# Optimization experiments

Hardware: AMD Instinct MI355X
Metric: run time of the kernel (lower is better)

The kernel has to match this reference:

```python
import jax, jax.numpy as jnp
import numpy as np

N_RAYS = 131072
N_SAMPLES = 128
FAR_DIST = 1e10  # matches tf constant 10000000000.0


def setup_inputs() -> dict:
    key = jax.random.key(0)
    k1, k2, k3, k4 = jax.random.split(key, 4)
    density = jax.random.normal(k1, (N_RAYS, N_SAMPLES), dtype=jnp.float32)
    color = jax.random.uniform(k2, (N_RAYS, N_SAMPLES, 3), dtype=jnp.float32)
    z_vals = jax.random.uniform(k3, (N_RAYS, N_SAMPLES), dtype=jnp.float32)
    rays_d = jax.random.normal(k4, (N_RAYS, 3), dtype=jnp.float32)
    return {"density": density, "color": color, "z_vals": z_vals, "rays_d": rays_d}


def reference(density, color, z_vals, rays_d):
    # dists between consecutive samples, last one padded with a huge value
    dists = z_vals[..., 1:] - z_vals[..., :-1]                      # [R, S-1]
    dists = jnp.concatenate(
        [dists, jnp.full_like(dists[..., :1], FAR_DIST)], axis=-1)  # [R, S]
    # scale by ray direction norm (broadcast over samples)
    dists = dists * jnp.linalg.norm(rays_d, axis=-1, keepdims=True)  # [R, S]
    # raw_noise_std = 0 -> no noise added (deterministic)
    alpha = 1.0 - jnp.exp(-jax.nn.relu(density) * dists)             # [R, S]
    # exclusive cumprod of transmittance
    t = jnp.cumprod(1.0 - alpha + 1e-10, axis=-1)                    # [R, S]
    trans = jnp.concatenate(
        [jnp.ones_like(t[..., :1]), t[..., :-1]], axis=-1)           # [R, S]
    weights = alpha * trans                                          # [R, S]
    rgb = jnp.sum(weights[..., None] * color, axis=-2)               # [R, 3]
    return rgb
```

## Files before the change

kernel.cpp:

```cpp
#include <hip/hip_runtime.h>

#define NS 128
#define FAR_DIST 1e10f

__global__ __launch_bounds__(256) void nerf_render_kernel(
    const float* __restrict__ density,
    const float* __restrict__ color,
    const float* __restrict__ z_vals,
    const float* __restrict__ rays_d,
    float* __restrict__ out,
    int n_rays)
{
    const int lane = threadIdx.x & 63;
    const int wave = threadIdx.x >> 6;
    const int ray  = blockIdx.x * 4 + wave;
    if (ray >= n_rays) return;

    const float* drow = density + (size_t)ray * NS;
    const float* zrow = z_vals  + (size_t)ray * NS;
    const float* crow = color   + (size_t)ray * NS * 3;

    float2 d2  = *reinterpret_cast<const float2*>(drow + 2 * lane);
    float2 z2  = *reinterpret_cast<const float2*>(zrow + 2 * lane);
    float2 c01 = *reinterpret_cast<const float2*>(crow + 6 * lane);
    float2 c23 = *reinterpret_cast<const float2*>(crow + 6 * lane + 2);
    float2 c45 = *reinterpret_cast<const float2*>(crow + 6 * lane + 4);

    float dx = rays_d[ray * 3 + 0];
    float dy = rays_d[ray * 3 + 1];
    float dz = rays_d[ray * 3 + 2];
    float nrm = sqrtf(dx * dx + dy * dy + dz * dz);

    float z_next = __shfl_down(z2.x, 1, 64);
    float dist0 = (z2.y - z2.x) * nrm;
    float dist1 = ((lane == 63) ? FAR_DIST : (z_next - z2.y)) * nrm;

    float a0 = 1.0f - expf(-fmaxf(d2.x, 0.0f) * dist0);
    float a1 = 1.0f - expf(-fmaxf(d2.y, 0.0f) * dist1);
    float f0 = 1.0f - a0 + 1e-10f;
    float f1 = 1.0f - a1 + 1e-10f;

    float p = f0 * f1;
    #pragma unroll
    for (int off = 1; off < 64; off <<= 1) {
        float up = __shfl_up(p, off, 64);
        if (lane >= off) p *= up;
    }
    float excl = __shfl_up(p, 1, 64);
    if (lane == 0) excl = 1.0f;

    float w0 = a0 * excl;
    float w1 = a1 * excl * f0;

    float r = w0 * c01.x + w1 * c23.y;
    float g = w0 * c01.y + w1 * c45.x;
    float b = w0 * c23.x + w1 * c45.y;

    #pragma unroll
    for (int off = 32; off >= 1; off >>= 1) {
        r += __shfl_xor(r, off, 64);
        g += __shfl_xor(g, off, 64);
        b += __shfl_xor(b, off, 64);
    }

    if (lane == 0) {
        out[ray * 3 + 0] = r;
        out[ray * 3 + 1] = g;
        out[ray * 3 + 2] = b;
    }
}

extern "C" void kernel_launch(void* const* d_in, const int* in_sizes, int n_in,
                              void* d_out, int out_size, void* d_ws, size_t ws_size,
                              hipStream_t stream) {
    const float* density = (const float*)d_in[0];
    const float* color   = (const float*)d_in[1];
    const float* z_vals  = (const float*)d_in[2];
    const float* rays_d  = (const float*)d_in[3];
    float* out = (float*)d_out;

    const int n_rays = in_sizes[3] / 3;
    const int blocks = (n_rays + 3) / 4;
    hipLaunchKernelGGL(nerf_render_kernel, dim3(blocks), dim3(256), 0, stream,
                       density, color, z_vals, rays_d, out, n_rays);
}
```

Before: 59.10 us.

## Use float4 loads with 32-lane groups per ray and fast exp

Each ray is now handled by a 32-lane group instead of a full 64-lane wave. Each lane processes four samples through float4 loads of density, z and color, so a block of 256 threads covers eight rays. The product scan and the reduction shrink to five shuffle steps, and expf is replaced with __expf. This cuts shuffle overhead and the number of memory instructions for a bandwidth-bound kernel, at the cost of lower-precision exponentials.

```diff
diff --git a/kernel.cpp b/kernel.cpp
--- a/kernel.cpp
+++ b/kernel.cpp
@@ -4,66 +4,73 @@
 #define FAR_DIST 1e10f
 
 __global__ __launch_bounds__(256) void nerf_render_kernel(
-    const float* __restrict__ density,
-    const float* __restrict__ color,
-    const float* __restrict__ z_vals,
-    const float* __restrict__ rays_d,
+    const float4* __restrict__ density4,
+    const float4* __restrict__ color4,
+    const float4* __restrict__ z4,
+    const float*  __restrict__ rays_d,
     float* __restrict__ out,
     int n_rays)
 {
-    const int lane = threadIdx.x & 63;
-    const int wave = threadIdx.x >> 6;
-    const int ray  = blockIdx.x * 4 + wave;
+    const int l   = threadIdx.x & 31;
+    const int grp = threadIdx.x >> 5;
+    const int ray = blockIdx.x * 8 + grp;
     if (ray >= n_rays) return;
 
-    const float* drow = density + (size_t)ray * NS;
-    const float* zrow = z_vals  + (size_t)ray * NS;
-    const float* crow = color   + (size_t)ray * NS * 3;
+    const float4 d  = density4[(size_t)ray * 32 + l];
+    const float4 z  = z4      [(size_t)ray * 32 + l];
+    const size_t cb = (size_t)ray * 96 + 3 * l;
+    const float4 c0 = color4[cb + 0];
+    const float4 c1 = color4[cb + 1];
+    const float4 c2 = color4[cb + 2];
 
-    float2 d2  = *reinterpret_cast<const float2*>(drow + 2 * lane);
-    float2 z2  = *reinterpret_cast<const float2*>(zrow + 2 * lane);
-    float2 c01 = *reinterpret_cast<const float2*>(crow + 6 * lane);
-    float2 c23 = *reinterpret_cast<const float2*>(crow + 6 * lane + 2);
-    float2 c45 = *reinterpret_cast<const float2*>(crow + 6 * lane + 4);
+    const float dx = rays_d[ray * 3 + 0];
+    const float dy = rays_d[ray * 3 + 1];
+    const float dz = rays_d[ray * 3 + 2];
+    const float nrm = sqrtf(dx * dx + dy * dy + dz * dz);
 
-    float dx = rays_d[ray * 3 + 0];
-    float dy = rays_d[ray * 3 + 1];
-    float dz = rays_d[ray * 3 + 2];
-    float nrm = sqrtf(dx * dx + dy * dy + dz * dz);
+    const float zn = __shfl_down(z.x, 1, 32);
+    const float dist0 = (z.y - z.x) * nrm;
+    const float dist1 = (z.z - z.y) * nrm;
+    const float dist2 = (z.w - z.z) * nrm;
+    const float dist3 = ((l == 31) ? FAR_DIST : (zn - z.w)) * nrm;
 
-    float z_next = __shfl_down(z2.x, 1, 64);
-    float dist0 = (z2.y - z2.x) * nrm;
-    float dist1 = ((lane == 63) ? FAR_DIST : (z_next - z2.y)) * nrm;
+    const float e0 = __expf(-fmaxf(d.x, 0.0f) * dist0);
+    const float e1 = __expf(-fmaxf(d.y, 0.0f) * dist1);
+    const float e2 = __expf(-fmaxf(d.z, 0.0f) * dist2);
+    const float e3 = __expf(-fmaxf(d.w, 0.0f) * dist3);
+    const float f0 = e0 + 1e-10f, f1 = e1 + 1e-10f;
+    const float f2 = e2 + 1e-10f, f3 = e3 + 1e-10f;
 
-    float a0 = 1.0f - expf(-fmaxf(d2.x, 0.0f) * dist0);
-    float a1 = 1.0f - expf(-fmaxf(d2.y, 0.0f) * dist1);
-    float f0 = 1.0f - a0 + 1e-10f;
-    float f1 = 1.0f - a1 + 1e-10f;
-
-    float p = f0 * f1;
-    #pragma unroll
-    for (int off = 1; off < 64; off <<= 1) {
-        float up = __shfl_up(p, off, 64);
-        if (lane >= off) p *= up;
-    }
-    float excl = __shfl_up(p, 1, 64);
-    if (lane == 0) excl = 1.0f;
-
-    float w0 = a0 * excl;
-    float w1 = a1 * excl * f0;
-
-    float r = w0 * c01.x + w1 * c23.y;
-    float g = w0 * c01.y + w1 * c45.x;
-    float b = w0 * c23.x + w1 * c45.y;
+    const float t1 = f0;
+    const float t2 = f0 * f1;
+    const float t3 = t2 * f2;
+    float p = t3 * f3;
 
     #pragma unroll
-    for (int off = 32; off >= 1; off >>= 1) {
-        r += __shfl_xor(r, off, 64);
-        g += __shfl_xor(g, off, 64);
-        b += __shfl_xor(b, off, 64);
+    for (int off = 1; off < 32; off <<= 1) {
+        const float up = __shfl_up(p, off, 32);
+        if (l >= off) p *= up;
+    }
+    float E = __shfl_up(p, 1, 32);
+    if (l == 0) E = 1.0f;
+
+    const float w0 = (1.0f - e0) * E;
+    const float w1 = (1.0f - e1) * E * t1;
+    const float w2 = (1.0f - e2) * E * t2;
+    const float w3 = (1.0f - e3) * E * t3;
+
+    float r = w0 * c0.x + w1 * c0.w + w2 * c1.z + w3 * c2.y;
+    float g = w0 * c0.y + w1 * c1.x + w2 * c1.w + w3 * c2.z;
+    float b = w0 * c0.z + w1 * c1.y + w2 * c2.x + w3 * c2.w;
+
+    #pragma unroll
+    for (int off = 16; off >= 1; off >>= 1) {
+        r += __shfl_xor(r, off, 32);
+        g += __shfl_xor(g, off, 32);
+        b += __shfl_xor(b, off, 32);
     }
 
-    if (lane == 0) {
+    if (l == 0) {
         out[ray * 3 + 0] = r;
         out[ray * 3 + 1] = g;
         out[ray * 3 + 2] = b;
@@ -73,14 +80,14 @@
 extern "C" void kernel_launch(void* const* d_in, const int* in_sizes, int n_in,
                               void* d_out, int out_size, void* d_ws, size_t ws_size,
                               hipStream_t stream) {
-    const float* density = (const float*)d_in[0];
-    const float* color   = (const float*)d_in[1];
-    const float* z_vals  = (const float*)d_in[2];
-    const float* rays_d  = (const float*)d_in[3];
+    const float4* density4 = (const float4*)d_in[0];
+    const float4* color4   = (const float4*)d_in[1];
+    const float4* z4       = (const float4*)d_in[2];
+    const float*  rays_d   = (const float*)d_in[3];
     float* out = (float*)d_out;
 
     const int n_rays = in_sizes[3] / 3;
-    const int blocks = (n_rays + 3) / 4;
+    const int blocks = (n_rays + 7) / 8;
     hipLaunchKernelGGL(nerf_render_kernel, dim3(blocks), dim3(256), 0, stream,
-                       density, color, z_vals, rays_d, out, n_rays);
+                       density4, color4, z4, rays_d, out, n_rays);
 }
```

New measurement: 58.59 us. About the same (-0.9%).
